# Performance work log

Hardware: AMD Instinct MI355X
Metric: run time of the kernel (lower is better)

## Reference

```python
import jax, jax.numpy as jnp
import numpy as np

CUTOFF = 5.2
BUCKETS_PER_CUTOFF = 1
BOX = 100.0
N_ATOMS = 100000
EXTRA_SPACE = 1e-5

# half-shell neighbor displacements: cartesian_prod(arange(-b,1)^3)[:-1] -> 7 vectors for b=1
_d1 = np.arange(-BUCKETS_PER_CUTOFF, 1)
DISPLACEMENTS = jnp.asarray(
    np.stack(np.meshgrid(_d1, _d1, _d1, indexing='ij'), axis=-1).reshape(-1, 3)[:-1],
    dtype=jnp.int32)  # (7, 3)
NUM_NEIGHBORS = DISPLACEMENTS.shape[0]


def setup_inputs() -> dict:
    key = jax.random.key(0)
    k1, _ = jax.random.split(key)
    # uniform in [0, 0.999*BOX) so fractional coordinates are strictly < 1
    coordinates = jax.random.uniform(k1, (1, N_ATOMS, 3), dtype=jnp.float32) * (BOX * 0.999)
    cell = jnp.eye(3, dtype=jnp.float32) * BOX
    return {"coordinates": coordinates, "cell": cell}


def _cumsum_from_zero(x):
    return jnp.concatenate([jnp.zeros((1,), x.dtype), jnp.cumsum(x[:-1])])


def reference(coordinates, cell):
    n_atoms = coordinates.shape[1]
    cell_diag = jnp.diagonal(cell)                       # (3,)
    bucket_length = CUTOFF / BUCKETS_PER_CUTOFF + EXTRA_SPACE
    grid = jnp.floor(cell_diag / bucket_length).astype(jnp.int32) + 1   # shape_buckets_grid (3,)
    total_buckets = int(grid[0] * grid[1] * grid[2])
    # faithful to source: [g1*g2, g1, 1]
    scaling = jnp.array([grid[1] * grid[2], grid[1], 1], dtype=jnp.int32)

    # fractionalize + main bucket vector/flat indices
    frac = coordinates / cell_diag.reshape(1, 1, -1)     # (1, N, 3)
    vec_idx = jnp.round(frac * (grid - 1).astype(frac.dtype)).astype(jnp.int32)  # (1, N, 3)
    flat = (vec_idx * scaling).sum(-1).reshape(-1)       # (N,) main_bucket_flat_index

    # image-index converters (stable argsort by bucket)
    imidx_from_atidx = jnp.argsort(flat)                 # jax argsort is stable
    atidx_from_imidx = jnp.argsort(imidx_from_atidx)

    # per-bucket counts / exclusive cumcounts
    counts = jnp.bincount(flat, length=total_buckets)
    cumcounts = _cumsum_from_zero(counts)
    max_in_bucket = int(counts.max())

    # ---- within-image pairs ----
    wp_idx = jnp.nonzero(counts > 1)[0]
    wp_count = counts[wp_idx]
    wp_cum = cumcounts[wp_idx]
    pu, pl = jnp.triu_indices(max_in_bucket, k=1)
    pairs = jnp.stack([pu, pl]).astype(jnp.int32)        # (2, P)
    # sort_along_row(row_for_sorting=1): key = upper + lower*max_in_bucket
    order = jnp.argsort(pairs[0] + pairs[1] * max_in_bucket)
    pairs = pairs[:, order]
    padded = pairs[None] + wp_cum.reshape(-1, 1, 1)      # (B, 2, P)
    padded = jnp.transpose(padded, (1, 0, 2)).reshape(2, -1)
    max_pairs = max_in_bucket * (max_in_bucket - 1) // 2
    mask = (jnp.arange(max_pairs)[None, :] < (wp_count * (wp_count - 1) // 2)[:, None]).reshape(-1)
    within_image_pairs = jnp.stack([padded[0][mask], padded[1][mask]])  # (2, n_pairs)

    # ---- between-image 'lower' indices ----
    neigh_vec = vec_idx[:, :, None, :] + DISPLACEMENTS   # (1, N, 7, 3)
    neigh_vec = jnp.mod(neigh_vec, grid)                 # pbc wrap of neighbor buckets
    neigh_flat = (neigh_vec * scaling).sum(-1)           # (1, N, 7)
    n_count = counts[neigh_flat]                         # (1, N, 7)
    n_cum = cumcounts[neigh_flat]                        # (1, N, 7)
    pad = jnp.broadcast_to(
        jnp.arange(max_in_bucket, dtype=n_cum.dtype).reshape(1, 1, 1, -1),
        (1, n_atoms, NUM_NEIGHBORS, max_in_bucket))      # (1, N, 7, M) -- dominant intermediate
    m = pad < n_count[..., None]
    lower_between = (pad + n_cum[..., None])[m]          # (n_between,)

    return within_image_pairs, lower_between, frac, imidx_from_atidx, atidx_from_imidx
```

## Files before the change

### kernel.cpp

```cpp
#include <hip/hip_runtime.h>
#include <hip/hip_bf16.h>

#define NB_MAX 8192
#define NTHR 256

__device__ __forceinline__ void get_grid(const float* __restrict__ cell,
                                         int& g0, int& g1, int& g2,
                                         float& d0, float& d1, float& d2) {
  d0 = cell[0]; d1 = cell[4]; d2 = cell[8];
  const float bl = (float)(5.2 + 1e-05);
  g0 = (int)floorf(d0 / bl) + 1;
  g1 = (int)floorf(d1 / bl) + 1;
  g2 = (int)floorf(d2 / bl) + 1;
}

__global__ void k_bucket_count(const float* __restrict__ coord,
                               const float* __restrict__ cell,
                               float* __restrict__ out_frac,
                               int* __restrict__ flat,
                               int* __restrict__ pv,
                               int* __restrict__ counts,
                               int* __restrict__ scalars, int n) {
  int a = blockIdx.x * blockDim.x + threadIdx.x;
  if (a >= n) return;
  int g0, g1, g2; float d0, d1, d2;
  get_grid(cell, g0, g1, g2, d0, d1, d2);
  if (a == 0) {
    scalars[8] = g0; scalars[9] = g1; scalars[10] = g2;
    scalars[11] = g1 * g2; scalars[12] = g0 * g1 * g2;
  }
  float x = coord[3 * a + 0], y = coord[3 * a + 1], z = coord[3 * a + 2];
  float fx = x / d0, fy = y / d1, fz = z / d2;
  out_frac[3 * a + 0] = fx;
  out_frac[3 * a + 1] = fy;
  out_frac[3 * a + 2] = fz;
  int v0 = (int)rintf(fx * (float)(g0 - 1));
  int v1 = (int)rintf(fy * (float)(g1 - 1));
  int v2 = (int)rintf(fz * (float)(g2 - 1));
  int b = v0 * (g1 * g2) + v1 * g1 + v2;
  flat[a] = b;
  pv[a] = (v0 << 20) | (v1 << 10) | v2;
  atomicAdd(&counts[b], 1);
}

__global__ __launch_bounds__(1024) void k_scan_buckets(
    const int* __restrict__ counts,
    int* __restrict__ cumc,
    int* __restrict__ pairoff,
    int* __restrict__ scalars) {
  int nb = scalars[12];
  const int T = 1024, IT = NB_MAX / 1024;
  __shared__ int wc[16], wp[16];
  int t = threadIdx.x;
  int lane = t & 63, wid = t >> 6;
  int base = t * IT;
  int cv[IT];
  int lc = 0, lp = 0;
  for (int i = 0; i < IT; ++i) {
    int idx = base + i;
    int c = (idx < nb) ? counts[idx] : 0;
    cv[i] = c;
    lc += c;
    lp += c * (c - 1) / 2;
  }
  int ic = lc, ip = lp;
  for (int off = 1; off < 64; off <<= 1) {
    int yc = __shfl_up(ic, off);
    int yp = __shfl_up(ip, off);
    if (lane >= off) { ic += yc; ip += yp; }
  }
  if (lane == 63) { wc[wid] = ic; wp[wid] = ip; }
  __syncthreads();
  if (wid == 0 && lane < 16) {
    int vc2 = wc[lane], vp2 = wp[lane];
    int sc2 = vc2, sp2 = vp2;
    for (int off = 1; off < 16; off <<= 1) {
      int yc = __shfl_up(sc2, off);
      int yp = __shfl_up(sp2, off);
      if (lane >= off) { sc2 += yc; sp2 += yp; }
    }
    wc[lane] = sc2 - vc2;
    wp[lane] = sp2 - vp2;
  }
  __syncthreads();
  int ec = wc[wid] + (ic - lc);
  int ep = wp[wid] + (ip - lp);
  for (int i = 0; i < IT; ++i) {
    int idx = base + i;
    if (idx < nb) { cumc[idx] = ec; pairoff[idx] = ep; }
    ec += cv[i];
    ep += cv[i] * (cv[i] - 1) / 2;
  }
  if (t == T - 1) scalars[0] = ep;
}

__global__ void k_scatter_runlen(const int* __restrict__ flat,
                                 const int* __restrict__ pv,
                                 const int* __restrict__ cumc,
                                 const int* __restrict__ counts,
                                 const int* __restrict__ scalars,
                                 int* __restrict__ fill,
                                 int* __restrict__ sorted,
                                 int* __restrict__ Sarr,
                                 int* __restrict__ blockpart, int n) {
  __shared__ int sm[NTHR];
  int t = threadIdx.x;
  int a = blockIdx.x * NTHR + t;
  int S = 0;
  if (a < n) {
    int b = flat[a];
    int pos = cumc[b] + atomicAdd(&fill[b], 1);
    sorted[pos] = a;
    int g0 = scalars[8], g1 = scalars[9], g2 = scalars[10], g12 = scalars[11];
    int p = pv[a];
    int v0 = p >> 20, v1 = (p >> 10) & 1023, v2 = p & 1023;
#pragma unroll
    for (int m = 0; m < 7; ++m) {
      int dx = ((m >> 2) & 1) ? 0 : -1;
      int dy = ((m >> 1) & 1) ? 0 : -1;
      int dz = (m & 1) ? 0 : -1;
      int nx = v0 + dx; if (nx < 0) nx += g0;
      int ny = v1 + dy; if (ny < 0) ny += g1;
      int nz = v2 + dz; if (nz < 0) nz += g2;
      S += counts[nx * g12 + ny * g1 + nz];
    }
    Sarr[a] = S;
  }
  sm[t] = S;
  __syncthreads();
  for (int off = NTHR / 2; off > 0; off >>= 1) {
    if (t < off) sm[t] += sm[t + off];
    __syncthreads();
  }
  if (t == 0) blockpart[blockIdx.x] = sm[0];
}

__global__ void k_sort_perm_pairs(const int* __restrict__ counts,
                                  const int* __restrict__ cumc,
                                  const int* __restrict__ pairoff,
                                  const int* __restrict__ scalars,
                                  int* __restrict__ sorted,
                                  float* __restrict__ out_im,
                                  float* __restrict__ out_at,
                                  float* __restrict__ out) {
  int lane = threadIdx.x & 63;
  int b = blockIdx.x * 4 + (threadIdx.x >> 6);
  int nb = scalars[12];
  if (b >= nb) return;
  int c = counts[b];
  if (c == 0) return;
  int s = cumc[b];
  if (c == 1) {
    if (lane == 0) {
      int a = sorted[s];
      out_im[s] = (float)a;
      out_at[a] = (float)s;
    }
    return;
  }
  if (c <= 64) {
    int val = (lane < c) ? sorted[s + lane] : 0x7fffffff;
    int rank = 0;
    for (int j = 0; j < c; ++j) {
      int other = __shfl(val, j);
      rank += (other < val) ? 1 : 0;
    }
    if (lane < c) {
      sorted[s + rank] = val;
      out_im[s + rank] = (float)val;
      out_at[val] = (float)(s + rank);
    }
  } else if (lane == 0) {
    for (int i = 1; i < c; ++i) {
      int key = sorted[s + i];
      int j = i - 1;
      while (j >= 0 && sorted[s + j] > key) {
        sorted[s + j + 1] = sorted[s + j];
        --j;
      }
      sorted[s + j + 1] = key;
    }
    for (int i = 0; i < c; ++i) {
      int a = sorted[s + i];
      out_im[s + i] = (float)a;
      out_at[a] = (float)(s + i);
    }
  }
  int off = pairoff[b];
  int P = scalars[0];
  int np = c * (c - 1) / 2;
  for (int k = lane; k < np; k += 64) {
    int l = (int)((1.0f + sqrtf(1.0f + 8.0f * (float)k)) * 0.5f);
    while (l * (l - 1) / 2 > k) --l;
    while ((l + 1) * l / 2 <= k) ++l;
    int u = k - l * (l - 1) / 2;
    out[off + k] = (float)(s + u);
    out[P + off + k] = (float)(s + l);
  }
}

__global__ __launch_bounds__(1024) void k_scan_partials(
    const int* __restrict__ blockpart,
    int* __restrict__ blockoff,
    int* __restrict__ scalars, int nblocks) {
  __shared__ int ws[16];
  int t = threadIdx.x;
  int lane = t & 63, wid = t >> 6;
  int v = (t < nblocks) ? blockpart[t] : 0;
  int iv = v;
  for (int off = 1; off < 64; off <<= 1) {
    int y = __shfl_up(iv, off);
    if (lane >= off) iv += y;
  }
  if (lane == 63) ws[wid] = iv;
  __syncthreads();
  if (wid == 0 && lane < 16) {
    int v2 = ws[lane], s2 = v2;
    for (int off = 1; off < 16; off <<= 1) {
      int y = __shfl_up(s2, off);
      if (lane >= off) s2 += y;
    }
    ws[lane] = s2 - v2;
  }
  __syncthreads();
  int excl = ws[wid] + (iv - v);
  blockoff[t] = excl;
  if (t == 1023) scalars[1] = excl + v;
}

__global__ void k_emit(const int* __restrict__ pv,
                       const int* __restrict__ counts,
                       const int* __restrict__ cumc,
                       const int* __restrict__ Sarr,
                       const int* __restrict__ blockoff,
                       const int* __restrict__ scalars,
                       float* __restrict__ out, int n) {
  __shared__ int ws[4];
  int t = threadIdx.x;
  int lane = t & 63, wid = t >> 6;
  int a = blockIdx.x * NTHR + t;
  int S = (a < n) ? Sarr[a] : 0;
  int iv = S;
  for (int off = 1; off < 64; off <<= 1) {
    int y = __shfl_up(iv, off);
    if (lane >= off) iv += y;
  }
  if (lane == 63) ws[wid] = iv;
  __syncthreads();
  if (wid == 0 && lane < 4) {
    int v2 = ws[lane], s2 = v2;
    for (int off = 1; off < 4; off <<= 1) {
      int y = __shfl_up(s2, off);
      if (lane >= off) s2 += y;
    }
    ws[lane] = s2 - v2;
  }
  __syncthreads();
  if (a >= n) return;
  int excl = ws[wid] + (iv - S);
  int g0 = scalars[8], g1 = scalars[9], g2 = scalars[10], g12 = scalars[11];
  int p = pv[a];
  int v0 = p >> 20, v1 = (p >> 10) & 1023, v2 = p & 1023;
  long base = 2L * (long)scalars[0] + (long)blockoff[blockIdx.x] + (long)excl;
  int k = 0;
#pragma unroll
  for (int m = 0; m < 7; ++m) {
    int dx = ((m >> 2) & 1) ? 0 : -1;
    int dy = ((m >> 1) & 1) ? 0 : -1;
    int dz = (m & 1) ? 0 : -1;
    int nx = v0 + dx; if (nx < 0) nx += g0;
    int ny = v1 + dy; if (ny < 0) ny += g1;
    int nz = v2 + dz; if (nz < 0) nz += g2;
    int nb_ = nx * g12 + ny * g1 + nz;
    int c = counts[nb_];
    int cum = cumc[nb_];
    for (int j = 0; j < c; ++j) {
      out[base + k] = (float)(cum + j);
      ++k;
    }
  }
}

extern "C" void kernel_launch(void* const* d_in, const int* in_sizes, int n_in,
                              void* d_out, int out_size, void* d_ws, size_t ws_size,
                              hipStream_t stream) {
  const float* coord = (const float*)d_in[0];
  const float* cell = (const float*)d_in[1];
  float* out = (float*)d_out;
  int n = in_sizes[0] / 3;

  int* W = (int*)d_ws;
  int* counts = W;
  int* fill = W + NB_MAX;
  int* scalars = W + 2 * NB_MAX;
  int* cumc = W + 2 * NB_MAX + 16;
  int* pairoff = cumc + NB_MAX;
  int* flat = pairoff + NB_MAX;
  int* pv = flat + n;
  int* sorted = pv + n;
  int* Sarr = sorted + n;
  int* blockpart = Sarr + n;
  int* blockoff = blockpart + 1024;

  float* out_frac = out + (out_size - 5 * n);
  float* out_im = out + (out_size - 2 * n);
  float* out_at = out + (out_size - n);

  int nblocks = (n + NTHR - 1) / NTHR;

  hipMemsetAsync(d_ws, 0, (size_t)(2 * NB_MAX + 16) * sizeof(int), stream);

  k_bucket_count<<<nblocks, NTHR, 0, stream>>>(coord, cell, out_frac, flat, pv, counts, scalars, n);
  k_scan_buckets<<<1, 1024, 0, stream>>>(counts, cumc, pairoff, scalars);
  k_scatter_runlen<<<nblocks, NTHR, 0, stream>>>(flat, pv, cumc, counts, scalars,
                                                 fill, sorted, Sarr, blockpart, n);
  k_sort_perm_pairs<<<NB_MAX / 4, 256, 0, stream>>>(counts, cumc, pairoff, scalars,
                                                    sorted, out_im, out_at, out);
  k_scan_partials<<<1, 1024, 0, stream>>>(blockpart, blockoff, scalars, nblocks);
  k_emit<<<nblocks, NTHR, 0, stream>>>(pv, counts, cumc, Sarr, blockoff, scalars, out, n);
}
```

Measured before the change: 132.5 us.

## Fuse block scans into scatter/sort kernels and emit neighbor indices with 16 lanes per atom

The per-block exclusive scan of neighbor counts moves into the scatter kernel, which now writes per-atom offsets directly. The scan of block partials is folded into an extra block of the sort/pairs kernel, which removes one kernel launch. The emit kernel now gives each atom 16 lanes that write strided, coalesced output, replacing a serial per-thread loop that wrote scattered addresses. The cost is 16x more threads doing redundant neighbor lookups, plus a 7-way segment select for every output element.

```diff
diff --git a/kernel.cpp b/kernel.cpp
--- a/kernel.cpp
+++ b/kernel.cpp
@@ -101,10 +101,11 @@
                                  const int* __restrict__ scalars,
                                  int* __restrict__ fill,
                                  int* __restrict__ sorted,
-                                 int* __restrict__ Sarr,
+                                 int* __restrict__ Oarr,
                                  int* __restrict__ blockpart, int n) {
-  __shared__ int sm[NTHR];
+  __shared__ int ws[4];
   int t = threadIdx.x;
+  int lane = t & 63, wid = t >> 6;
   int a = blockIdx.x * NTHR + t;
   int S = 0;
   if (a < n) {
@@ -124,15 +125,25 @@
       int nz = v2 + dz; if (nz < 0) nz += g2;
       S += counts[nx * g12 + ny * g1 + nz];
     }
-    Sarr[a] = S;
-  }
-  sm[t] = S;
+  }
+  int iv = S;
+  for (int off = 1; off < 64; off <<= 1) {
+    int y = __shfl_up(iv, off);
+    if (lane >= off) iv += y;
+  }
+  if (lane == 63) ws[wid] = iv;
   __syncthreads();
-  for (int off = NTHR / 2; off > 0; off >>= 1) {
-    if (t < off) sm[t] += sm[t + off];
-    __syncthreads();
-  }
-  if (t == 0) blockpart[blockIdx.x] = sm[0];
+  if (wid == 0 && lane < 4) {
+    int v2 = ws[lane], s2 = v2;
+    for (int off = 1; off < 4; off <<= 1) {
+      int y = __shfl_up(s2, off);
+      if (lane >= off) s2 += y;
+    }
+    ws[lane] = s2 - v2;
+    if (lane == 3) blockpart[blockIdx.x] = s2;
+  }
+  __syncthreads();
+  if (a < n) Oarr[a] = ws[wid] + (iv - S);
 }
 
 __global__ void k_sort_perm_pairs(const int* __restrict__ counts,
@@ -142,9 +153,45 @@
                                   int* __restrict__ sorted,
                                   float* __restrict__ out_im,
                                   float* __restrict__ out_at,
-                                  float* __restrict__ out) {
-  int lane = threadIdx.x & 63;
-  int b = blockIdx.x * 4 + (threadIdx.x >> 6);
+                                  float* __restrict__ out,
+                                  const int* __restrict__ blockpart,
+                                  int* __restrict__ blockoff, int nblocks) {
+  __shared__ int shm[4];
+  int t = threadIdx.x;
+  int lane = t & 63, wid = t >> 6;
+  if (blockIdx.x == gridDim.x - 1) {
+    int base = t * 4;
+    int cv[4];
+    int ls = 0;
+    for (int i = 0; i < 4; ++i) {
+      int v = (base + i < nblocks) ? blockpart[base + i] : 0;
+      cv[i] = v;
+      ls += v;
+    }
+    int il = ls;
+    for (int off = 1; off < 64; off <<= 1) {
+      int y = __shfl_up(il, off);
+      if (lane >= off) il += y;
+    }
+    if (lane == 63) shm[wid] = il;
+    __syncthreads();
+    if (wid == 0 && lane < 4) {
+      int v2 = shm[lane], s2 = v2;
+      for (int off = 1; off < 4; off <<= 1) {
+        int y = __shfl_up(s2, off);
+        if (lane >= off) s2 += y;
+      }
+      shm[lane] = s2 - v2;
+    }
+    __syncthreads();
+    int e = shm[wid] + (il - ls);
+    for (int i = 0; i < 4; ++i) {
+      blockoff[base + i] = e;
+      e += cv[i];
+    }
+    return;
+  }
+  int b = blockIdx.x * 4 + wid;
   int nb = scalars[12];
   if (b >= nb) return;
   int c = counts[b];
@@ -199,70 +246,23 @@
   }
 }
 
-__global__ __launch_bounds__(1024) void k_scan_partials(
-    const int* __restrict__ blockpart,
-    int* __restrict__ blockoff,
-    int* __restrict__ scalars, int nblocks) {
-  __shared__ int ws[16];
-  int t = threadIdx.x;
-  int lane = t & 63, wid = t >> 6;
-  int v = (t < nblocks) ? blockpart[t] : 0;
-  int iv = v;
-  for (int off = 1; off < 64; off <<= 1) {
-    int y = __shfl_up(iv, off);
-    if (lane >= off) iv += y;
-  }
-  if (lane == 63) ws[wid] = iv;
-  __syncthreads();
-  if (wid == 0 && lane < 16) {
-    int v2 = ws[lane], s2 = v2;
-    for (int off = 1; off < 16; off <<= 1) {
-      int y = __shfl_up(s2, off);
-      if (lane >= off) s2 += y;
-    }
-    ws[lane] = s2 - v2;
-  }
-  __syncthreads();
-  int excl = ws[wid] + (iv - v);
-  blockoff[t] = excl;
-  if (t == 1023) scalars[1] = excl + v;
-}
-
-__global__ void k_emit(const int* __restrict__ pv,
-                       const int* __restrict__ counts,
-                       const int* __restrict__ cumc,
-                       const int* __restrict__ Sarr,
-                       const int* __restrict__ blockoff,
-                       const int* __restrict__ scalars,
-                       float* __restrict__ out, int n) {
-  __shared__ int ws[4];
-  int t = threadIdx.x;
-  int lane = t & 63, wid = t >> 6;
-  int a = blockIdx.x * NTHR + t;
-  int S = (a < n) ? Sarr[a] : 0;
-  int iv = S;
-  for (int off = 1; off < 64; off <<= 1) {
-    int y = __shfl_up(iv, off);
-    if (lane >= off) iv += y;
-  }
-  if (lane == 63) ws[wid] = iv;
-  __syncthreads();
-  if (wid == 0 && lane < 4) {
-    int v2 = ws[lane], s2 = v2;
-    for (int off = 1; off < 4; off <<= 1) {
-      int y = __shfl_up(s2, off);
-      if (lane >= off) s2 += y;
-    }
-    ws[lane] = s2 - v2;
-  }
-  __syncthreads();
+__global__ void k_emit16(const int* __restrict__ pv,
+                         const int* __restrict__ counts,
+                         const int* __restrict__ cumc,
+                         const int* __restrict__ Oarr,
+                         const int* __restrict__ blockoff,
+                         const int* __restrict__ scalars,
+                         float* __restrict__ out, int n) {
+  int gt = blockIdx.x * blockDim.x + threadIdx.x;
+  int a = gt >> 4;
+  int l16 = gt & 15;
   if (a >= n) return;
-  int excl = ws[wid] + (iv - S);
   int g0 = scalars[8], g1 = scalars[9], g2 = scalars[10], g12 = scalars[11];
   int p = pv[a];
   int v0 = p >> 20, v1 = (p >> 10) & 1023, v2 = p & 1023;
-  long base = 2L * (long)scalars[0] + (long)blockoff[blockIdx.x] + (long)excl;
-  int k = 0;
+  int segs[8];
+  int cums[7];
+  segs[0] = 0;
 #pragma unroll
   for (int m = 0; m < 7; ++m) {
     int dx = ((m >> 2) & 1) ? 0 : -1;
@@ -272,12 +272,18 @@
     int ny = v1 + dy; if (ny < 0) ny += g1;
     int nz = v2 + dz; if (nz < 0) nz += g2;
     int nb_ = nx * g12 + ny * g1 + nz;
-    int c = counts[nb_];
-    int cum = cumc[nb_];
-    for (int j = 0; j < c; ++j) {
-      out[base + k] = (float)(cum + j);
-      ++k;
-    }
+    cums[m] = cumc[nb_];
+    segs[m + 1] = segs[m] + counts[nb_];
+  }
+  int S = segs[7];
+  long base = 2L * (long)scalars[0] + (long)blockoff[a >> 8] + (long)Oarr[a];
+  for (int q = l16; q < S; q += 16) {
+    int v = cums[0] + q;
+#pragma unroll
+    for (int m = 1; m < 7; ++m) {
+      if (q >= segs[m]) v = cums[m] + (q - segs[m]);
+    }
+    out[base + q] = (float)v;
   }
 }
 
@@ -298,8 +304,8 @@
   int* flat = pairoff + NB_MAX;
   int* pv = flat + n;
   int* sorted = pv + n;
-  int* Sarr = sorted + n;
-  int* blockpart = Sarr + n;
+  int* Oarr = sorted + n;
+  int* blockpart = Oarr + n;
   int* blockoff = blockpart + 1024;
 
   float* out_frac = out + (out_size - 5 * n);
@@ -313,9 +319,10 @@
   k_bucket_count<<<nblocks, NTHR, 0, stream>>>(coord, cell, out_frac, flat, pv, counts, scalars, n);
   k_scan_buckets<<<1, 1024, 0, stream>>>(counts, cumc, pairoff, scalars);
   k_scatter_runlen<<<nblocks, NTHR, 0, stream>>>(flat, pv, cumc, counts, scalars,
-                                                 fill, sorted, Sarr, blockpart, n);
-  k_sort_perm_pairs<<<NB_MAX / 4, 256, 0, stream>>>(counts, cumc, pairoff, scalars,
-                                                    sorted, out_im, out_at, out);
-  k_scan_partials<<<1, 1024, 0, stream>>>(blockpart, blockoff, scalars, nblocks);
-  k_emit<<<nblocks, NTHR, 0, stream>>>(pv, counts, cumc, Sarr, blockoff, scalars, out, n);
-}
+                                                 fill, sorted, Oarr, blockpart, n);
+  k_sort_perm_pairs<<<NB_MAX / 4 + 1, 256, 0, stream>>>(counts, cumc, pairoff, scalars,
+                                                        sorted, out_im, out_at, out,
+                                                        blockpart, blockoff, nblocks);
+  k_emit16<<<(n * 16 + 255) / 256, 256, 0, stream>>>(pv, counts, cumc, Oarr, blockoff,
+                                                     scalars, out, n);
+}
```

Result: faster. 115.7 us (-12.7%).
